# Performance work log

Measured on AMD Instinct MI355X. Metric: run time of the kernel, lower is better.

Reference implementation:

```python
import jax, jax.numpy as jnp
import numpy as np

TAIL_BOUND = 3.0
MIN_BIN_W = 1e-3
MIN_BIN_H = 1e-3
MIN_DERIV = 1e-3


def _rq_spline_fwd(x, uw, uh, us):
    # unconstrained rational-quadratic spline (Durkan et al., 'linear' tails)
    # x: [N, C]; uw, uh: [C, B]; us: [C, B-1]
    C, B = uw.shape
    dt = x.dtype
    inside = (x >= -TAIL_BOUND) & (x <= TAIL_BOUND)
    xc = jnp.clip(x, -TAIL_BOUND, TAIL_BOUND)

    widths = MIN_BIN_W + (1.0 - MIN_BIN_W * B) * jax.nn.softmax(uw, axis=-1)
    cumw = jnp.concatenate([jnp.zeros((C, 1), dt), jnp.cumsum(widths, -1)], -1)
    cumw = 2.0 * TAIL_BOUND * cumw - TAIL_BOUND
    cumw = cumw.at[:, 0].set(-TAIL_BOUND).at[:, -1].set(TAIL_BOUND)
    widths = cumw[:, 1:] - cumw[:, :-1]

    heights = MIN_BIN_H + (1.0 - MIN_BIN_H * B) * jax.nn.softmax(uh, axis=-1)
    cumh = jnp.concatenate([jnp.zeros((C, 1), dt), jnp.cumsum(heights, -1)], -1)
    cumh = 2.0 * TAIL_BOUND * cumh - TAIL_BOUND
    cumh = cumh.at[:, 0].set(-TAIL_BOUND).at[:, -1].set(TAIL_BOUND)
    heights = cumh[:, 1:] - cumh[:, :-1]

    # boundary derivative logits -> softplus(const) = 1 - MIN_DERIV
    const = float(np.log(np.expm1(1.0 - MIN_DERIV)))
    ud = jnp.concatenate([jnp.full((C, 1), const, dt), us,
                          jnp.full((C, 1), const, dt)], -1)
    derivs = MIN_DERIV + jax.nn.softplus(ud)  # [C, B+1]

    # searchsorted on bin x-edges (eps shift on last edge, as in reference impl)
    edges = cumw.at[:, -1].add(1e-6)
    idx = jnp.clip(jnp.sum(xc[:, :, None] >= edges[None, :, :], -1) - 1, 0, B - 1)  # [N, C]

    ci = jnp.arange(C)[None, :]
    xk = cumw[ci, idx]
    wk = widths[ci, idx]
    yk = cumh[ci, idx]
    hk = heights[ci, idx]
    dk = derivs[ci, idx]
    dk1 = derivs[ci, idx + 1]
    delta = hk / wk

    theta = (xc - xk) / wk
    t1m = theta * (1.0 - theta)
    num = hk * (delta * theta * theta + dk * t1m)
    den = delta + (dk + dk1 - 2.0 * delta) * t1m
    y = yk + num / den
    dnum = delta * delta * (dk1 * theta * theta + 2.0 * delta * t1m
                            + dk * (1.0 - theta) * (1.0 - theta))
    logdet = jnp.log(dnum) - 2.0 * jnp.log(den)

    # identity (log-det 0) outside the interval
    return jnp.where(inside, y, x), jnp.where(inside, logdet, jnp.zeros_like(logdet))


def setup_inputs() -> dict:
    key = jax.random.key(0)
    ks = jax.random.split(key, 6)
    N, L, C, B = 1000000, 8, 8, 32
    return {
        "x": jax.random.normal(ks[0], (N,), jnp.float32),
        "w": jax.random.normal(ks[1], (L, C, B), jnp.float32),
        "h": jax.random.normal(ks[2], (L, C, B), jnp.float32),
        "s": jax.random.normal(ks[3], (L, C, B - 1), jnp.float32),
        "bias": jax.random.normal(ks[4], (L + 1, C), jnp.float32),
        "log_scale": jax.random.normal(ks[5], (L + 1, C), jnp.float32),
    }


def reference(x, w, h, s, bias, log_scale):
    L, C = w.shape[0], w.shape[1]
    z = jnp.broadcast_to(x[:, None], (x.shape[0], C))
    log_j = jnp.zeros_like(z)
    for step in range(L):
        z = (z - bias[step]) * jnp.exp(-log_scale[step])
        z, ld = _rq_spline_fwd(z, w[step], h[step], s[step])
        log_j = log_j + ld - log_scale[step]
    z = (z - bias[L]) * jnp.exp(-log_scale[L])
    return z, log_j - log_scale[L]
```

## Files before the change

### kernel.cpp

```cpp
#include <hip/hip_runtime.h>
#include <hip/hip_bf16.h>


#define TB 3.0f
#define NB 32
#define NC 8
#define NL 8
#define LN2 0.69314718055994530942f

#define GX0 -6.5f
#define GX1 6.5f
#define TZ 0.5f
#define TL 0.5f

#define PT_FLOATS (64 * 99)
#define GP_FLOATS (PT_FLOATS + 72 + 72 + 8)
#define GP_BYTES  (GP_FLOATS * 4)
#define TAB_OFF   26112
#define CAP 256

__device__ __forceinline__ float softplusf(float v) {
    return fmaxf(v, 0.f) + log1pf(expf(-fabsf(v)));
}

__device__ __forceinline__ unsigned short f2h(float f) {
    _Float16 h = (_Float16)f;
    unsigned short u;
    __builtin_memcpy(&u, &h, 2);
    return u;
}
__device__ __forceinline__ float h2f(unsigned short u) {
    _Float16 h;
    __builtin_memcpy(&h, &u, 2);
    return (float)h;
}

__device__ __forceinline__ int bsearch32(const float* __restrict__ E, float xc) {
    int i = (xc >= E[16]) ? 16 : 0;
    i += (xc >= E[i + 8]) ? 8 : 0;
    i += (xc >= E[i + 4]) ? 4 : 0;
    i += (xc >= E[i + 2]) ? 2 : 0;
    i += (xc >= E[i + 1]) ? 1 : 0;
    return i;
}

__device__ __forceinline__ void spline_eval(const float* __restrict__ Tlc,
                                            float zc, float& zo, float& ldo) {
    const float* E  = Tlc;
    const float* Hc = Tlc + 33;
    const float* Dv = Tlc + 66;

    float xc = fminf(fmaxf(zc, -TB), TB);
    int i = bsearch32(E, xc);

    float xk  = E[i],  xk1 = E[i + 1];
    float yk  = Hc[i], yk1 = Hc[i + 1];
    float dk  = Dv[i], dk1 = Dv[i + 1];

    float wk    = xk1 - xk;
    float hk    = yk1 - yk;
    float invw  = __builtin_amdgcn_rcpf(wk);
    float delta = hk * invw;
    float th    = (xc - xk) * invw;
    float omt   = 1.f - th;
    float t1m   = th * omt;
    float th2   = th * th;

    float num    = hk * fmaf(delta, th2, dk * t1m);
    float den    = fmaf(fmaf(-2.f, delta, dk + dk1), t1m, delta);
    float invden = __builtin_amdgcn_rcpf(den);
    float y      = fmaf(num, invden, yk);

    float dt    = delta * t1m;
    float inner = fmaf(dk1, th2, fmaf(dk, omt * omt, dt + dt));
    float dnum  = (delta * delta) * inner;
    float r  = dnum * invden * invden;
    float ld = LN2 * __builtin_amdgcn_logf(r);

    bool inside = (zc >= -TB) && (zc <= TB);
    zo  = inside ? y : zc;
    ldo = inside ? ld : 0.f;
}

__device__ __forceinline__ void exact_chain(const float* __restrict__ T,
                                            float xv, int c,
                                            float& zout, float& lout) {
    const float* ScT = T + PT_FLOATS;
    const float* BbT = ScT + 72;
    const float* LJT = BbT + 72;
    float zc = xv;
    float lacc = LJT[c];
#pragma unroll 1
    for (int l = 0; l < NL; ++l) {
        zc = (zc - BbT[l * 8 + c]) * ScT[l * 8 + c];
        float ld;
        spline_eval(T + (l * 8 + c) * 99, zc, zc, ld);
        lacc += ld;
    }
    zout = (zc - BbT[NL * 8 + c]) * ScT[NL * 8 + c];
    lout = lacc;
}

extern "C" __global__ void __launch_bounds__(256)
build_tables(const float* __restrict__ w, const float* __restrict__ h,
             const float* __restrict__ s, const float* __restrict__ bias,
             const float* __restrict__ lsc, float* __restrict__ gparam)
{
    __shared__ float T[PT_FLOATS];
    __shared__ float Sc[72], Bb[72], LJ[8];

    const int tid = threadIdx.x;

    if (tid < 64) {
        const int l = tid >> 3, c = tid & 7;
        float* cw = &T[tid * 99];
        const float* wr = w + (l * NC + c) * NB;
        float m = wr[0];
        for (int b = 1; b < NB; ++b) m = fmaxf(m, wr[b]);
        float sum = 0.f;
        for (int b = 0; b < NB; ++b) sum += expf(wr[b] - m);
        float inv = 1.f / sum;
        float acc = 0.f;
        cw[0] = -TB;
        for (int b = 0; b < NB; ++b) {
            acc += 1e-3f + (1.f - 1e-3f * NB) * (expf(wr[b] - m) * inv);
            cw[b + 1] = 6.f * acc - 3.f;
        }
        cw[NB] = TB;
    } else if (tid < 128) {
        const int t = tid - 64;
        float* ch = &T[t * 99 + 33];
        const int l = t >> 3, c = t & 7;
        const float* hr = h + (l * NC + c) * NB;
        float m = hr[0];
        for (int b = 1; b < NB; ++b) m = fmaxf(m, hr[b]);
        float sum = 0.f;
        for (int b = 0; b < NB; ++b) sum += expf(hr[b] - m);
        float inv = 1.f / sum;
        float acc = 0.f;
        ch[0] = -TB;
        for (int b = 0; b < NB; ++b) {
            acc += 1e-3f + (1.f - 1e-3f * NB) * (expf(hr[b] - m) * inv);
            ch[b + 1] = 6.f * acc - 3.f;
        }
        ch[NB] = TB;
    } else if (tid < 192) {
        const int t = tid - 128;
        const int l = t >> 3, c = t & 7;
        float* dv = &T[t * 99 + 66];
        const float* sr = s + (l * NC + c) * (NB - 1);
        const float cst = logf(expm1f(1.f - 1e-3f));
        const float dbound = 1e-3f + softplusf(cst);
        dv[0]  = dbound;
        dv[NB] = dbound;
        for (int k = 0; k < NB - 1; ++k)
            dv[k + 1] = 1e-3f + softplusf(sr[k]);
    }
    if (tid < 72) { Sc[tid] = expf(-lsc[tid]); Bb[tid] = bias[tid]; }
    if (tid < 8) {
        float a = 0.f;
        for (int l = 0; l <= NL; ++l) a += lsc[l * NC + tid];
        LJ[tid] = -a;
    }
    __syncthreads();

    for (int k = tid; k < PT_FLOATS; k += 256) gparam[k] = T[k];
    if (tid < 72) gparam[PT_FLOATS + tid]       = Sc[tid];
    if (tid < 72) gparam[PT_FLOATS + 72 + tid]  = Bb[tid];
    if (tid < 8)  gparam[PT_FLOATS + 144 + tid] = LJ[tid];
}

extern "C" __global__ void __launch_bounds__(256)
grid_eval(const float* __restrict__ gparam, char* __restrict__ tabb,
          int G, float dx)
{
    __shared__ float T[GP_FLOATS];
    __shared__ unsigned short ZL[256 * 16];
    for (int k = threadIdx.x; k < GP_FLOATS; k += 256) T[k] = gparam[k];
    __syncthreads();
    const float* ScT = T + PT_FLOATS;
    const float* BbT = ScT + 72;
    const float* LJT = BbT + 72;

    const int t  = threadIdx.x;
    const int p0 = blockIdx.x * 255;
    const int i  = min(p0 + t, G - 1);

    const float xv = fmaf((float)i, dx, GX0);
    float z[NC], lj[NC];
#pragma unroll
    for (int c = 0; c < NC; ++c) { z[c] = xv; lj[c] = LJT[c]; }

#pragma unroll 1
    for (int l = 0; l < NL; ++l) {
        const float* Tl = T + l * NC * 99;
#pragma unroll
        for (int c = 0; c < NC; ++c) {
            float u = (z[c] - BbT[l * 8 + c]) * ScT[l * 8 + c];
            float zo, ld;
            spline_eval(Tl + c * 99, u, zo, ld);
            z[c] = zo;
            lj[c] += ld;
        }
    }
    unsigned short zh[NC], lh[NC];
#pragma unroll
    for (int c = 0; c < NC; ++c) {
        z[c] = (z[c] - BbT[NL * 8 + c]) * ScT[NL * 8 + c];
        zh[c] = f2h(z[c]);
        lh[c] = f2h(lj[c]);
        ZL[t * 16 + c]     = zh[c];
        ZL[t * 16 + 8 + c] = lh[c];
    }
    __syncthreads();

    const int r = p0 + t;
    if (t < 255 && r <= G - 2) {
        ushort4* rowp = (ushort4*)(tabb + (size_t)r * 64);
#pragma unroll
        for (int c = 0; c < NC; ++c) {
            const float zn  = h2f(ZL[(t + 1) * 16 + c]);
            const float ljn = h2f(ZL[(t + 1) * 16 + 8 + c]);
            ushort4 v;
            v.x = zh[c]; v.y = f2h(zn - h2f(zh[c]));
            v.z = lh[c]; v.w = f2h(ljn - h2f(lh[c]));
            rowp[c] = v;
        }
    }
}

extern "C" __global__ void __launch_bounds__(256)
interp_kernel(const float* __restrict__ x, const char* __restrict__ tabb,
              const float* __restrict__ gparam, float* __restrict__ out,
              int N, int G, float dx, float invdx)
{
    __shared__ float T[GP_FLOATS];
    __shared__ float xbuf[256];
    __shared__ unsigned short pairs[CAP];
    __shared__ float resZ[CAP], resL[CAP];
    __shared__ unsigned wsum[4];

    const int tid  = threadIdx.x;
    const int n    = blockIdx.x * 256 + tid;
    const int lane = tid & 63;
    const int wloc = tid >> 6;
    const bool active = (n < N);

    float xv = 0.f;
    if (active) xv = x[n];
    xbuf[tid] = xv;

    float z[NC], lj[NC];
    int flags = 0;
    if (active) {
        int i = (int)floorf((xv - GX0) * invdx);
        const bool oor = !(xv > GX0 && xv < GX1);
        i = min(max(i, 0), G - 2);
        const float t = (xv - fmaf((float)i, dx, GX0)) * invdx;

        const float4* rp = (const float4*)(tabb + (size_t)i * 64);
        union { float4 q[4]; unsigned int u[16]; } R;
        R.q[0] = rp[0]; R.q[1] = rp[1]; R.q[2] = rp[2]; R.q[3] = rp[3];
#pragma unroll
        for (int c = 0; c < NC; ++c) {
            const unsigned a = R.u[2 * c], b = R.u[2 * c + 1];
            const float z0 = h2f((unsigned short)a);
            const float dz = h2f((unsigned short)(a >> 16));
            const float l0 = h2f((unsigned short)b);
            const float dl = h2f((unsigned short)(b >> 16));
            z[c]  = fmaf(t, dz, z0);
            lj[c] = fmaf(t, dl, l0);
            if (fabsf(dz) > TZ || fabsf(dl) > TL) flags |= (1 << c);
        }
        if (oor) flags = 0xff;
    }

    unsigned long long m[NC];
    unsigned wtot = 0;
#pragma unroll
    for (int c = 0; c < NC; ++c) {
        m[c] = __ballot((flags >> c) & 1);
        wtot += (unsigned)__popcll(m[c]);
    }
    if (lane == 0) wsum[wloc] = wtot;
    __syncthreads();

    unsigned woff = 0, btot = 0;
#pragma unroll
    for (int j = 0; j < 4; ++j) {
        const unsigned v = wsum[j];
        if (j < wloc) woff += v;
        btot += v;
    }
    const unsigned long long lowmask = (1ull << lane) - 1ull;
    {
        unsigned basec = 0;
#pragma unroll
        for (int c = 0; c < NC; ++c) {
            if ((flags >> c) & 1) {
                const unsigned idx = woff + basec + (unsigned)__popcll(m[c] & lowmask);
                if (idx < CAP) pairs[idx] = (unsigned short)((tid << 3) | c);
            }
            basec += (unsigned)__popcll(m[c]);
        }
    }
    if (btot > 0) {
        for (int k = tid; k < GP_FLOATS; k += 256) T[k] = gparam[k];
    }
    __syncthreads();

    const unsigned pcnt = min(btot, (unsigned)CAP);
    for (unsigned k = tid; k < pcnt; k += 256) {
        const unsigned pr = pairs[k];
        const int stid = (int)(pr >> 3), c = (int)(pr & 7u);
        float zo, lo;
        exact_chain(T, xbuf[stid], c, zo, lo);
        resZ[k] = zo; resL[k] = lo;
    }
    __syncthreads();

    if (active && flags) {
        unsigned basec = 0;
#pragma unroll
        for (int c = 0; c < NC; ++c) {
            if ((flags >> c) & 1) {
                const unsigned idx = woff + basec + (unsigned)__popcll(m[c] & lowmask);
                if (idx < CAP) {
                    z[c] = resZ[idx]; lj[c] = resL[idx];
                } else {
                    exact_chain(T, xv, c, z[c], lj[c]);
                }
            }
            basec += (unsigned)__popcll(m[c]);
        }
    }

    if (active) {
        float4* oz = (float4*)(out + (size_t)n * NC);
        oz[0] = make_float4(z[0], z[1], z[2], z[3]);
        oz[1] = make_float4(z[4], z[5], z[6], z[7]);
        float4* ol = (float4*)(out + (size_t)N * NC + (size_t)n * NC);
        ol[0] = make_float4(lj[0], lj[1], lj[2], lj[3]);
        ol[1] = make_float4(lj[4], lj[5], lj[6], lj[7]);
    }
}

extern "C" __global__ void __launch_bounds__(256)
flow_kernel(const float* __restrict__ x, const float* __restrict__ w,
            const float* __restrict__ h, const float* __restrict__ s,
            const float* __restrict__ bias, const float* __restrict__ lsc,
            float* __restrict__ out, int N)
{
    __shared__ float T[PT_FLOATS];
    __shared__ float Bb[NL + 1][NC];
    __shared__ float Sc[NL + 1][NC];
    __shared__ float LJC[NC];

    const int tid = threadIdx.x;
    if (tid < 64) {
        const int l = tid >> 3, c = tid & 7;
        float* cw = &T[tid * 99];
        {
            const float* wr = w + (l * NC + c) * NB;
            float m = wr[0];
            for (int b = 1; b < NB; ++b) m = fmaxf(m, wr[b]);
            float sum = 0.f;
            for (int b = 0; b < NB; ++b) sum += expf(wr[b] - m);
            float inv = 1.f / sum;
            float acc = 0.f;
            cw[0] = -TB;
            for (int b = 0; b < NB; ++b) {
                acc += 1e-3f + (1.f - 1e-3f * NB) * (expf(wr[b] - m) * inv);
                cw[b + 1] = 6.f * acc - 3.f;
            }
            cw[NB] = TB;
        }
        {
            float* ch = cw + 33;
            const float* hr = h + (l * NC + c) * NB;
            float m = hr[0];
            for (int b = 1; b < NB; ++b) m = fmaxf(m, hr[b]);
            float sum = 0.f;
            for (int b = 0; b < NB; ++b) sum += expf(hr[b] - m);
            float inv = 1.f / sum;
            float acc = 0.f;
            ch[0] = -TB;
            for (int b = 0; b < NB; ++b) {
                acc += 1e-3f + (1.f - 1e-3f * NB) * (expf(hr[b] - m) * inv);
                ch[b + 1] = 6.f * acc - 3.f;
            }
            ch[NB] = TB;
        }
        {
            float* dv = cw + 66;
            const float* sr = s + (l * NC + c) * (NB - 1);
            const float cst = logf(expm1f(1.f - 1e-3f));
            const float dbound = 1e-3f + softplusf(cst);
            dv[0]  = dbound;
            dv[NB] = dbound;
            for (int k = 0; k < NB - 1; ++k)
                dv[k + 1] = 1e-3f + softplusf(sr[k]);
        }
    }
    if (tid < (NL + 1) * NC) {
        const int l = tid >> 3, c = tid & 7;
        Bb[l][c] = bias[tid];
        Sc[l][c] = expf(-lsc[tid]);
    }
    if (tid < NC) {
        float a = 0.f;
        for (int l = 0; l <= NL; ++l) a += lsc[l * NC + tid];
        LJC[tid] = -a;
    }
    __syncthreads();

    const int n = blockIdx.x * 256 + tid;
    if (n >= N) return;
    const float xv = x[n];
    float z[NC], lj[NC];
#pragma unroll
    for (int c = 0; c < NC; ++c) { z[c] = xv; lj[c] = LJC[c]; }
#pragma unroll 1
    for (int l = 0; l < NL; ++l) {
        const float* Tl = &T[l * NC * 99];
#pragma unroll
        for (int c = 0; c < NC; ++c) {
            float zc = (z[c] - Bb[l][c]) * Sc[l][c];
            float zo, ld;
            spline_eval(Tl + c * 99, zc, zo, ld);
            z[c] = zo;
            lj[c] += ld;
        }
    }
#pragma unroll
    for (int c = 0; c < NC; ++c) z[c] = (z[c] - Bb[NL][c]) * Sc[NL][c];

    float4* oz = (float4*)(out + (size_t)n * NC);
    oz[0] = make_float4(z[0], z[1], z[2], z[3]);
    oz[1] = make_float4(z[4], z[5], z[6], z[7]);
    float4* ol = (float4*)(out + (size_t)N * NC + (size_t)n * NC);
    ol[0] = make_float4(lj[0], lj[1], lj[2], lj[3]);
    ol[1] = make_float4(lj[4], lj[5], lj[6], lj[7]);
}

extern "C" void kernel_launch(void* const* d_in, const int* in_sizes, int n_in,
                              void* d_out, int out_size, void* d_ws, size_t ws_size,
                              hipStream_t stream) {
    const float* x    = (const float*)d_in[0];
    const float* w    = (const float*)d_in[1];
    const float* h    = (const float*)d_in[2];
    const float* s    = (const float*)d_in[3];
    const float* bias = (const float*)d_in[4];
    const float* lsc  = (const float*)d_in[5];
    float* out = (float*)d_out;
    const int N = in_sizes[0];

    int G = 65536;
    while (G > 2048 && ((size_t)TAB_OFF + (size_t)G * 64) > ws_size)
        G >>= 1;
    const size_t need = (size_t)TAB_OFF + (size_t)G * 64;

    if (need <= ws_size) {
        char* basep = (char*)d_ws;
        float* gparam = (float*)basep;
        char*  tabb   = basep + TAB_OFF;

        const float dx = (GX1 - GX0) / (float)(G - 1);
        const int gblocks = (G - 1 + 254) / 255;
        build_tables<<<1, 256, 0, stream>>>(w, h, s, bias, lsc, gparam);
        grid_eval<<<gblocks, 256, 0, stream>>>(gparam, tabb, G, dx);
        interp_kernel<<<(N + 255) / 256, 256, 0, stream>>>(
            x, tabb, gparam, out, N, G, dx, 1.f / dx);
    } else {
        flow_kernel<<<(N + 255) / 256, 256, 0, stream>>>(
            x, w, h, s, bias, lsc, out, N);
    }
}
```

Before: 63.91 us.

## Remap interp kernel threads to (point, channel) pairs for coalesced table access

Each thread now handles one channel for eight points, not all eight channels of one point. Table reads become 8-byte loads per channel, and the output stores are fully coalesced scalar stores in which adjacent lanes write adjacent channels. The flagged-pair compaction is redone per group with per-wave counts, so lanes in a wave share the exact-chain fallback work more evenly. In exchange, x is read redundantly by eight threads, there are more ballots, and stores are scalar rather than float4.

Result: slower. 74.61 us (+16.7%).

```diff
diff --git a/kernel.cpp b/kernel.cpp
--- a/kernel.cpp
+++ b/kernel.cpp
@@ -236,72 +236,74 @@
 {
     __shared__ float T[GP_FLOATS];
     __shared__ float xbuf[256];
-    __shared__ unsigned short pairs[CAP];
+    __shared__ unsigned short pool[CAP];
     __shared__ float resZ[CAP], resL[CAP];
-    __shared__ unsigned wsum[4];
-
-    const int tid  = threadIdx.x;
-    const int n    = blockIdx.x * 256 + tid;
-    const int lane = tid & 63;
-    const int wloc = tid >> 6;
-    const bool active = (n < N);
-
-    float xv = 0.f;
-    if (active) xv = x[n];
-    xbuf[tid] = xv;
-
-    float z[NC], lj[NC];
-    int flags = 0;
-    if (active) {
-        int i = (int)floorf((xv - GX0) * invdx);
-        const bool oor = !(xv > GX0 && xv < GX1);
-        i = min(max(i, 0), G - 2);
-        const float t = (xv - fmaf((float)i, dx, GX0)) * invdx;
-
-        const float4* rp = (const float4*)(tabb + (size_t)i * 64);
-        union { float4 q[4]; unsigned int u[16]; } R;
-        R.q[0] = rp[0]; R.q[1] = rp[1]; R.q[2] = rp[2]; R.q[3] = rp[3];
-#pragma unroll
-        for (int c = 0; c < NC; ++c) {
-            const unsigned a = R.u[2 * c], b = R.u[2 * c + 1];
-            const float z0 = h2f((unsigned short)a);
-            const float dz = h2f((unsigned short)(a >> 16));
-            const float l0 = h2f((unsigned short)b);
-            const float dl = h2f((unsigned short)(b >> 16));
-            z[c]  = fmaf(t, dz, z0);
-            lj[c] = fmaf(t, dl, l0);
-            if (fabsf(dz) > TZ || fabsf(dl) > TL) flags |= (1 << c);
-        }
-        if (oor) flags = 0xff;
-    }
-
-    unsigned long long m[NC];
-    unsigned wtot = 0;
-#pragma unroll
-    for (int c = 0; c < NC; ++c) {
-        m[c] = __ballot((flags >> c) & 1);
-        wtot += (unsigned)__popcll(m[c]);
-    }
-    if (lane == 0) wsum[wloc] = wtot;
-    __syncthreads();
-
-    unsigned woff = 0, btot = 0;
-#pragma unroll
-    for (int j = 0; j < 4; ++j) {
-        const unsigned v = wsum[j];
-        if (j < wloc) woff += v;
-        btot += v;
-    }
+    __shared__ unsigned wgcnt[8][4];
+
+    const int tid   = threadIdx.x;
+    const int c     = tid & 7;
+    const int pbase = tid >> 3;
+    const int lane  = tid & 63;
+    const int wloc  = tid >> 6;
+    const int P0    = blockIdx.x * 256;
+
+    float zv[8], lv[8], xr[8];
+    unsigned long long mg[8];
+    unsigned char myf[8];
+
+#pragma unroll
+    for (int g = 0; g < 8; ++g) {
+        const int pl = g * 32 + pbase;
+        const int p  = P0 + pl;
+        const bool active = (p < N);
+        float xv = 0.f, z0 = 0.f, dz = 0.f, l0 = 0.f, dl = 0.f;
+        bool flag = false;
+        float t = 0.f;
+        if (active) {
+            xv = x[p];
+            int i = (int)floorf((xv - GX0) * invdx);
+            const bool oor = !(xv > GX0 && xv < GX1);
+            i = min(max(i, 0), G - 2);
+            t = (xv - fmaf((float)i, dx, GX0)) * invdx;
+            const uint2 ab = *(const uint2*)(tabb + (size_t)i * 64 + c * 8);
+            z0 = h2f((unsigned short)ab.x);
+            dz = h2f((unsigned short)(ab.x >> 16));
+            l0 = h2f((unsigned short)ab.y);
+            dl = h2f((unsigned short)(ab.y >> 16));
+            flag = oor || (fabsf(dz) > TZ) || (fabsf(dl) > TL);
+        }
+        zv[g] = fmaf(t, dz, z0);
+        lv[g] = fmaf(t, dl, l0);
+        xr[g] = xv;
+        myf[g] = flag ? 1 : 0;
+        mg[g] = __ballot(flag);
+        if (lane == 0) wgcnt[g][wloc] = (unsigned)__popcll(mg[g]);
+        if (c == 0) xbuf[pl] = xv;
+    }
+    __syncthreads();
+
+    unsigned btot = 0;
+    unsigned goff[8];
+#pragma unroll
+    for (int g = 0; g < 8; ++g) {
+        unsigned og = btot;
+        unsigned wo = 0;
+#pragma unroll
+        for (int j = 0; j < 4; ++j) {
+            const unsigned v = wgcnt[g][j];
+            if (j < wloc) wo += v;
+            btot += v;
+        }
+        goff[g] = og + wo;
+    }
+
     const unsigned long long lowmask = (1ull << lane) - 1ull;
-    {
-        unsigned basec = 0;
-#pragma unroll
-        for (int c = 0; c < NC; ++c) {
-            if ((flags >> c) & 1) {
-                const unsigned idx = woff + basec + (unsigned)__popcll(m[c] & lowmask);
-                if (idx < CAP) pairs[idx] = (unsigned short)((tid << 3) | c);
-            }
-            basec += (unsigned)__popcll(m[c]);
+#pragma unroll
+    for (int g = 0; g < 8; ++g) {
+        if (myf[g]) {
+            const unsigned idx = goff[g] + (unsigned)__popcll(mg[g] & lowmask);
+            if (idx < CAP)
+                pool[idx] = (unsigned short)(((g * 32 + pbase) << 3) | c);
         }
     }
     if (btot > 0) {
@@ -311,37 +313,33 @@
 
     const unsigned pcnt = min(btot, (unsigned)CAP);
     for (unsigned k = tid; k < pcnt; k += 256) {
-        const unsigned pr = pairs[k];
-        const int stid = (int)(pr >> 3), c = (int)(pr & 7u);
+        const unsigned pr = pool[k];
         float zo, lo;
-        exact_chain(T, xbuf[stid], c, zo, lo);
+        exact_chain(T, xbuf[pr >> 3], (int)(pr & 7u), zo, lo);
         resZ[k] = zo; resL[k] = lo;
     }
     __syncthreads();
 
-    if (active && flags) {
-        unsigned basec = 0;
-#pragma unroll
-        for (int c = 0; c < NC; ++c) {
-            if ((flags >> c) & 1) {
-                const unsigned idx = woff + basec + (unsigned)__popcll(m[c] & lowmask);
-                if (idx < CAP) {
-                    z[c] = resZ[idx]; lj[c] = resL[idx];
-                } else {
-                    exact_chain(T, xv, c, z[c], lj[c]);
-                }
+#pragma unroll
+    for (int g = 0; g < 8; ++g) {
+        if (myf[g]) {
+            const unsigned idx = goff[g] + (unsigned)__popcll(mg[g] & lowmask);
+            if (idx < CAP) {
+                zv[g] = resZ[idx]; lv[g] = resL[idx];
+            } else {
+                exact_chain(T, xr[g], c, zv[g], lv[g]);
             }
-            basec += (unsigned)__popcll(m[c]);
-        }
-    }
-
-    if (active) {
-        float4* oz = (float4*)(out + (size_t)n * NC);
-        oz[0] = make_float4(z[0], z[1], z[2], z[3]);
-        oz[1] = make_float4(z[4], z[5], z[6], z[7]);
-        float4* ol = (float4*)(out + (size_t)N * NC + (size_t)n * NC);
-        ol[0] = make_float4(lj[0], lj[1], lj[2], lj[3]);
-        ol[1] = make_float4(lj[4], lj[5], lj[6], lj[7]);
+        }
+    }
+
+#pragma unroll
+    for (int g = 0; g < 8; ++g) {
+        const int pl = g * 32 + pbase;
+        const int p  = P0 + pl;
+        if (p < N) {
+            out[(size_t)p * NC + c] = zv[g];
+            out[(size_t)N * NC + (size_t)p * NC + c] = lv[g];
+        }
     }
 }
 
```

## Split grid_eval channels across thread halves and simplify fallback compaction to per-point

Applied to the files above, without the earlier changes.

grid_eval now assigns 4 channels per thread, with two thread halves covering 127 grid points per block. This doubles the block count and halves the per-thread serial spline work, which should shorten the grid-building stage. interp_kernel replaces per-(point,channel) ballot compaction with a single per-point flag, so any flagged point gets all 8 channels recomputed exactly. The pool is capped at 64 points, and any overflow falls back to a serial in-thread chain. This cuts the ballot and popcount work but can recompute channels that did not need it.

After: 61.72 us, median of 2. -3.4%, faster.

```diff
diff --git a/kernel.cpp b/kernel.cpp
--- a/kernel.cpp
+++ b/kernel.cpp
@@ -17,7 +17,7 @@
 #define GP_FLOATS (PT_FLOATS + 72 + 72 + 8)
 #define GP_BYTES  (GP_FLOATS * 4)
 #define TAB_OFF   26112
-#define CAP 256
+#define CAPP 64
 
 __device__ __forceinline__ float softplusf(float v) {
     return fmaxf(v, 0.f) + log1pf(expf(-fabsf(v)));
@@ -175,55 +175,59 @@
           int G, float dx)
 {
     __shared__ float T[GP_FLOATS];
-    __shared__ unsigned short ZL[256 * 16];
+    __shared__ unsigned short ZL[128 * 16];
     for (int k = threadIdx.x; k < GP_FLOATS; k += 256) T[k] = gparam[k];
     __syncthreads();
     const float* ScT = T + PT_FLOATS;
     const float* BbT = ScT + 72;
     const float* LJT = BbT + 72;
 
-    const int t  = threadIdx.x;
-    const int p0 = blockIdx.x * 255;
-    const int i  = min(p0 + t, G - 1);
+    const int pl = threadIdx.x & 127;
+    const int c0 = (threadIdx.x >> 7) * 4;
+    const int p0 = blockIdx.x * 127;
+    const int i  = min(p0 + pl, G - 1);
 
     const float xv = fmaf((float)i, dx, GX0);
-    float z[NC], lj[NC];
-#pragma unroll
-    for (int c = 0; c < NC; ++c) { z[c] = xv; lj[c] = LJT[c]; }
+    float z[4], lj[4];
+#pragma unroll
+    for (int cc = 0; cc < 4; ++cc) { z[cc] = xv; lj[cc] = LJT[c0 + cc]; }
 
 #pragma unroll 1
     for (int l = 0; l < NL; ++l) {
         const float* Tl = T + l * NC * 99;
 #pragma unroll
-        for (int c = 0; c < NC; ++c) {
-            float u = (z[c] - BbT[l * 8 + c]) * ScT[l * 8 + c];
+        for (int cc = 0; cc < 4; ++cc) {
+            const int c = c0 + cc;
+            float u = (z[cc] - BbT[l * 8 + c]) * ScT[l * 8 + c];
             float zo, ld;
             spline_eval(Tl + c * 99, u, zo, ld);
-            z[c] = zo;
-            lj[c] += ld;
-        }
-    }
-    unsigned short zh[NC], lh[NC];
-#pragma unroll
-    for (int c = 0; c < NC; ++c) {
-        z[c] = (z[c] - BbT[NL * 8 + c]) * ScT[NL * 8 + c];
-        zh[c] = f2h(z[c]);
-        lh[c] = f2h(lj[c]);
-        ZL[t * 16 + c]     = zh[c];
-        ZL[t * 16 + 8 + c] = lh[c];
-    }
-    __syncthreads();
-
-    const int r = p0 + t;
-    if (t < 255 && r <= G - 2) {
+            z[cc] = zo;
+            lj[cc] += ld;
+        }
+    }
+    unsigned short zh[4], lh[4];
+#pragma unroll
+    for (int cc = 0; cc < 4; ++cc) {
+        const int c = c0 + cc;
+        z[cc] = (z[cc] - BbT[NL * 8 + c]) * ScT[NL * 8 + c];
+        zh[cc] = f2h(z[cc]);
+        lh[cc] = f2h(lj[cc]);
+        ZL[pl * 16 + c]     = zh[cc];
+        ZL[pl * 16 + 8 + c] = lh[cc];
+    }
+    __syncthreads();
+
+    const int r = p0 + pl;
+    if (pl < 127 && r <= G - 2) {
         ushort4* rowp = (ushort4*)(tabb + (size_t)r * 64);
 #pragma unroll
-        for (int c = 0; c < NC; ++c) {
-            const float zn  = h2f(ZL[(t + 1) * 16 + c]);
-            const float ljn = h2f(ZL[(t + 1) * 16 + 8 + c]);
+        for (int cc = 0; cc < 4; ++cc) {
+            const int c = c0 + cc;
+            const float zn  = h2f(ZL[(pl + 1) * 16 + c]);
+            const float ljn = h2f(ZL[(pl + 1) * 16 + 8 + c]);
             ushort4 v;
-            v.x = zh[c]; v.y = f2h(zn - h2f(zh[c]));
-            v.z = lh[c]; v.w = f2h(ljn - h2f(lh[c]));
+            v.x = zh[cc]; v.y = f2h(zn - h2f(zh[cc]));
+            v.z = lh[cc]; v.w = f2h(ljn - h2f(lh[cc]));
             rowp[c] = v;
         }
     }
@@ -236,9 +240,9 @@
 {
     __shared__ float T[GP_FLOATS];
     __shared__ float xbuf[256];
-    __shared__ unsigned short pairs[CAP];
-    __shared__ float resZ[CAP], resL[CAP];
-    __shared__ unsigned wsum[4];
+    __shared__ unsigned char pool[CAPP];
+    __shared__ float resZ[CAPP * 8], resL[CAPP * 8];
+    __shared__ unsigned wcnt[4];
 
     const int tid  = threadIdx.x;
     const int n    = blockIdx.x * 256 + tid;
@@ -251,7 +255,7 @@
     xbuf[tid] = xv;
 
     float z[NC], lj[NC];
-    int flags = 0;
+    bool pflag = false;
     if (active) {
         int i = (int)floorf((xv - GX0) * invdx);
         const bool oor = !(xv > GX0 && xv < GX1);
@@ -261,6 +265,7 @@
         const float4* rp = (const float4*)(tabb + (size_t)i * 64);
         union { float4 q[4]; unsigned int u[16]; } R;
         R.q[0] = rp[0]; R.q[1] = rp[1]; R.q[2] = rp[2]; R.q[3] = rp[3];
+        int flags = 0;
 #pragma unroll
         for (int c = 0; c < NC; ++c) {
             const unsigned a = R.u[2 * c], b = R.u[2 * c + 1];
@@ -270,68 +275,51 @@
             const float dl = h2f((unsigned short)(b >> 16));
             z[c]  = fmaf(t, dz, z0);
             lj[c] = fmaf(t, dl, l0);
-            if (fabsf(dz) > TZ || fabsf(dl) > TL) flags |= (1 << c);
-        }
-        if (oor) flags = 0xff;
-    }
-
-    unsigned long long m[NC];
-    unsigned wtot = 0;
-#pragma unroll
-    for (int c = 0; c < NC; ++c) {
-        m[c] = __ballot((flags >> c) & 1);
-        wtot += (unsigned)__popcll(m[c]);
-    }
-    if (lane == 0) wsum[wloc] = wtot;
+            if (fabsf(dz) > TZ || fabsf(dl) > TL) flags = 1;
+        }
+        pflag = oor || (flags != 0);
+    }
+
+    const unsigned long long m = __ballot(pflag);
+    if (lane == 0) wcnt[wloc] = (unsigned)__popcll(m);
     __syncthreads();
 
     unsigned woff = 0, btot = 0;
 #pragma unroll
     for (int j = 0; j < 4; ++j) {
-        const unsigned v = wsum[j];
+        const unsigned v = wcnt[j];
         if (j < wloc) woff += v;
         btot += v;
     }
-    const unsigned long long lowmask = (1ull << lane) - 1ull;
-    {
-        unsigned basec = 0;
-#pragma unroll
-        for (int c = 0; c < NC; ++c) {
-            if ((flags >> c) & 1) {
-                const unsigned idx = woff + basec + (unsigned)__popcll(m[c] & lowmask);
-                if (idx < CAP) pairs[idx] = (unsigned short)((tid << 3) | c);
-            }
-            basec += (unsigned)__popcll(m[c]);
-        }
-    }
+    const unsigned idx = woff +
+        (unsigned)__popcll(m & ((1ull << lane) - 1ull));
+    if (pflag && idx < CAPP) pool[idx] = (unsigned char)tid;
     if (btot > 0) {
         for (int k = tid; k < GP_FLOATS; k += 256) T[k] = gparam[k];
     }
     __syncthreads();
 
-    const unsigned pcnt = min(btot, (unsigned)CAP);
-    for (unsigned k = tid; k < pcnt; k += 256) {
-        const unsigned pr = pairs[k];
-        const int stid = (int)(pr >> 3), c = (int)(pr & 7u);
+    const unsigned pcnt = min(btot, (unsigned)CAPP);
+    for (unsigned k = tid; k < pcnt * 8u; k += 256) {
+        const int pt = (int)pool[k >> 3];
+        const int cc = (int)(k & 7u);
         float zo, lo;
-        exact_chain(T, xbuf[stid], c, zo, lo);
+        exact_chain(T, xbuf[pt], cc, zo, lo);
         resZ[k] = zo; resL[k] = lo;
     }
     __syncthreads();
 
-    if (active && flags) {
-        unsigned basec = 0;
-#pragma unroll
-        for (int c = 0; c < NC; ++c) {
-            if ((flags >> c) & 1) {
-                const unsigned idx = woff + basec + (unsigned)__popcll(m[c] & lowmask);
-                if (idx < CAP) {
-                    z[c] = resZ[idx]; lj[c] = resL[idx];
-                } else {
-                    exact_chain(T, xv, c, z[c], lj[c]);
-                }
+    if (pflag) {
+        if (idx < CAPP) {
+#pragma unroll
+            for (int c = 0; c < NC; ++c) {
+                z[c]  = resZ[idx * 8 + c];
+                lj[c] = resL[idx * 8 + c];
             }
-            basec += (unsigned)__popcll(m[c]);
+        } else {
+#pragma unroll 1
+            for (int c = 0; c < NC; ++c)
+                exact_chain(T, xv, c, z[c], lj[c]);
         }
     }
 
@@ -466,7 +454,7 @@
         char*  tabb   = basep + TAB_OFF;
 
         const float dx = (GX1 - GX0) / (float)(G - 1);
-        const int gblocks = (G - 1 + 254) / 255;
+        const int gblocks = (G - 1 + 126) / 127;
         build_tables<<<1, 256, 0, stream>>>(w, h, s, bias, lsc, gparam);
         grid_eval<<<gblocks, 256, 0, stream>>>(gparam, tabb, G, dx);
         interp_kernel<<<(N + 255) / 256, 256, 0, stream>>>(
```
